# Performance work log

Measured on AMD Instinct MI355X. Metric: run time of the kernel, lower is better.

The kernel has to match this reference:

```python
import jax, jax.numpy as jnp
import numpy as np

B, T, D, U = 128, 2048, 256, 512
ALPHA = 0.001


def hard_sigmoid(x):
    return jnp.clip(0.2 * x + 0.5, 0.0, 1.0)


def setup_inputs() -> dict:
    key = jax.random.key(0)
    k1, k2, k3 = jax.random.split(key, 3)
    x = jax.random.normal(k1, (B, T, D), dtype=jnp.float32)
    h0 = jnp.zeros((B, U), dtype=jnp.float32)
    c0 = jnp.zeros((B, U), dtype=jnp.float32)
    t0 = jnp.zeros((B, U), dtype=jnp.float32)
    # glorot-ish kernels
    kernel = jax.random.normal(k2, (D, 4 * U), dtype=jnp.float32) * (1.0 / np.sqrt(D))
    recurrent_kernel = jax.random.normal(k3, (U, 4 * U), dtype=jnp.float32) * (1.0 / np.sqrt(U))
    # bias zeros with forget-gate slice = 1 (unit_forget_bias)
    bias = jnp.zeros((4 * U,), dtype=jnp.float32).at[U:2 * U].set(1.0)
    # timegate: rows = period ~ U(10,100), shift ~ U(0,1000), r_on = 0.05
    rng = np.random.RandomState(0)
    timegate_kernel = jnp.asarray(
        np.vstack((rng.uniform(10, 100, U), rng.uniform(0, 1000, U), np.zeros(U) + 0.05)),
        dtype=jnp.float32)
    return {"x": x, "h0": h0, "c0": c0, "t0": t0, "kernel": kernel,
            "recurrent_kernel": recurrent_kernel, "bias": bias,
            "timegate_kernel": timegate_kernel}


def reference(x, h0, c0, t0, kernel, recurrent_kernel, bias, timegate_kernel):
    period = timegate_kernel[0]  # [U]
    shift = timegate_kernel[1]   # [U]
    r_on = timegate_kernel[2]    # [U]

    def step(carry, x_t):
        h, c, t = carry
        t = t + 1.0
        # fused gate pre-activations: [B, 4U]
        z = x_t @ kernel + h @ recurrent_kernel + bias
        zi, zf, zc, zo = jnp.split(z, 4, axis=-1)
        i = hard_sigmoid(zi)
        f = hard_sigmoid(zf)
        c_hat = f * c + i * jnp.tanh(zc)
        o = hard_sigmoid(zo)
        h_hat = o * jnp.tanh(c_hat)
        # phased time gate
        phi = (t - shift - period * jnp.floor((t - shift) / period)) / period
        k = jnp.where(phi <= r_on * 0.5, 2.0 * phi / r_on,
                      jnp.where(phi <= r_on, 2.0 - 2.0 * phi / r_on, ALPHA * phi))
        c_new = k * c_hat + (1.0 - k) * c
        h_new = k * h_hat + (1.0 - k) * h
        return (h_new, c_new, t), h_new

    xs = jnp.swapaxes(x, 0, 1)  # [T, B, D]
    (_, _, _), hs = jax.lax.scan(step, (h0, c0, t0), xs)
    return jnp.swapaxes(hs, 0, 1)  # [B, T, U]
```

## Files before the change

kernel.cpp:

```cpp
#include <hip/hip_runtime.h>
#include <hip/hip_bf16.h>
#include <math.h>

#define B_ 128
#define T_ 2048
#define D_ 256
#define U_ 512
#define G4_ 2048
#define KT_ 768
#define ALPHA_ 0.001f

#define NGROUP 8
#define GB 16
#define NSLICE 32
#define SU 16
#define NWG (NGROUP*NSLICE)
#define NTH 256
#define BU (B_*U_)

typedef __attribute__((ext_vector_type(8))) short bf16x8;
typedef __attribute__((ext_vector_type(4))) float f32x4;
typedef __attribute__((ext_vector_type(4))) int i32x4;
typedef __attribute__((ext_vector_type(2))) int i32x2;
typedef __attribute__((ext_vector_type(4))) unsigned short us4;

#define OFF_WT 0
#define OFF_H32 (G4_*KT_*2)
#define OFF_CNT (OFF_H32 + 2*BU*4)
#define CNT_DW (NGROUP*64)

__device__ __forceinline__ unsigned short f2b(float f) {
  unsigned u = __builtin_bit_cast(unsigned, f);
  u += 0x7fffu + ((u >> 16) & 1u);
  return (unsigned short)(u >> 16);
}

__device__ __forceinline__ float ftanh(float v) {
  v = fminf(fmaxf(v, -15.f), 15.f);
  float e = __expf(2.f * v);
  return (e - 1.f) * __builtin_amdgcn_rcpf(e + 1.f);
}

__global__ void prep_kernel(const float* __restrict__ kern,
                            const float* __restrict__ rker,
                            const float* __restrict__ h0,
                            unsigned short* __restrict__ wt,
                            unsigned* __restrict__ h32,
                            unsigned* __restrict__ cnt) {
  int idx = blockIdx.x * blockDim.x + threadIdx.x;
  int stride = gridDim.x * blockDim.x;
  for (int i = idx; i < G4_ * KT_; i += stride) {
    int col = i / KT_, k = i - col * KT_;
    float v = (k < U_) ? rker[(size_t)k * G4_ + col]
                       : kern[(size_t)(k - U_) * G4_ + col];
    wt[i] = f2b(v);
  }
  for (int i = idx; i < BU; i += stride) {
    h32[i] = ((unsigned)f2b(h0[i]) << 16);
    h32[BU + i] = 0xFFFFu;
  }
  for (int i = idx; i < CNT_DW; i += stride) cnt[i] = 0u;
}

#define LOAD8()                                                        \
  asm volatile(                                                        \
      "global_load_dwordx4 %0, %8, off sc0 sc1\n\t"                    \
      "global_load_dwordx4 %1, %8, off offset:1024 sc0 sc1\n\t"        \
      "global_load_dwordx4 %2, %8, off offset:2048 sc0 sc1\n\t"        \
      "global_load_dwordx4 %3, %8, off offset:3072 sc0 sc1\n\t"        \
      "global_load_dwordx4 %4, %9, off sc0 sc1\n\t"                    \
      "global_load_dwordx4 %5, %9, off offset:1024 sc0 sc1\n\t"        \
      "global_load_dwordx4 %6, %9, off offset:2048 sc0 sc1\n\t"        \
      "global_load_dwordx4 %7, %9, off offset:3072 sc0 sc1"            \
      : "=&v"(v0), "=&v"(v1), "=&v"(v2), "=&v"(v3),                    \
        "=&v"(v4), "=&v"(v5), "=&v"(v6), "=&v"(v7)                     \
      : "v"(ppoll), "v"(ppoll2));                                      \
  __builtin_amdgcn_sched_barrier(0)

#define FENCE8()                                                       \
  asm volatile("s_waitcnt vmcnt(0)"                                    \
      : "+v"(v0), "+v"(v1), "+v"(v2), "+v"(v3),                        \
        "+v"(v4), "+v"(v5), "+v"(v6), "+v"(v7));                       \
  __builtin_amdgcn_sched_barrier(0)

#define CKV(vv) ((((unsigned)(vv)[0] ^ tgv) & 0xffffu) |               \
                 (((unsigned)(vv)[1] ^ tgv) & 0xffffu) |               \
                 (((unsigned)(vv)[2] ^ tgv) & 0xffffu) |               \
                 (((unsigned)(vv)[3] ^ tgv) & 0xffffu))

#define PK(lo, hi) (int)(((unsigned)(hi) & 0xffff0000u) | ((unsigned)(lo) >> 16))

#define PACK2(vv, k)                                                         \
  { const int r_ = 4 * wv + ((k) >> 1);                                      \
    const int ba_ = (r_ * 1024 + (((k) & 1) << 9) + 8 * ln) ^ ((r_ & 7) << 4); \
    i32x2 d_ = { PK((vv)[0], (vv)[1]), PK((vv)[2], (vv)[3]) };               \
    *(i32x2*)(hdst + ba_) = d_; }

__global__ __launch_bounds__(NTH, 1) void plstm_kernel(
    const float* __restrict__ x, const float* __restrict__ h0,
    const float* __restrict__ c0, const float* __restrict__ t0,
    const float* __restrict__ bias, const float* __restrict__ tg,
    const unsigned short* __restrict__ wt,
    unsigned* h32, unsigned* cnt, float* __restrict__ out) {
  const int wg = blockIdx.x;
  const int g = wg & 7, sl = wg >> 3;
  const int b0 = g * GB, u0 = sl * SU;
  const int tid = threadIdx.x;
  const int wave = tid >> 6, lane = tid & 63;

  __shared__ unsigned short h_lds[2][GB * U_];
  __shared__ unsigned short x_lds[2][GB * D_];
  __shared__ float z_lds[2][GB][68];
  __shared__ unsigned wgarr[4];

  bf16x8 br[16], bx[8];
  {
    const int kr0 = (lane >> 4) * 8;
    const int col0 = wave * U_ + u0 + (lane & 15);
    const unsigned short* w0 = wt + (size_t)col0 * KT_;
#pragma unroll
    for (int kt = 0; kt < 16; ++kt) br[kt] = *(const bf16x8*)(w0 + kt * 32 + kr0);
#pragma unroll
    for (int kt = 0; kt < 8; ++kt)  bx[kt] = *(const bf16x8*)(w0 + U_ + kt * 32 + kr0);
  }
  const float bias_l = bias[wave * U_ + u0 + (lane & 15)];

  const int srow = tid >> 4;
  const int j = tid & 15;
  const int bb = b0 + srow;
  const int uu = u0 + j;
  float c_st = c0[bb * U_ + uu];
  float h_st = h0[bb * U_ + uu];
  const float t_0 = t0[bb * U_ + uu];
  const float per = tg[uu];
  const float shf = tg[U_ + uu];
  const float ron = tg[2 * U_ + uu];

  const int arow = lane & 15;
  const int koff = (lane >> 4) * 16;
  const int swzA = (arow & 7) << 4;
  const int swzR = (srow & 7) << 4;
  const int wv = wave, ln = lane;

  auto stage_x = [&](int t, int buf) {
    const int f0 = j * 16;
    const float* xp = x + ((size_t)bb * T_ + t) * D_ + f0;
    char* base = (char*)&x_lds[buf][0];
#pragma unroll
    for (int q = 0; q < 4; ++q) {
      float4 v = *(const float4*)(xp + q * 4);
      us4 pk = { f2b(v.x), f2b(v.y), f2b(v.z), f2b(v.w) };
      *(us4*)(base + ((srow * 512 + (f0 + q * 4) * 2) ^ swzR)) = pk;
    }
  };

  stage_x(0, 0);
  stage_x(1, 1);
  if (tid < 4) wgarr[tid] = 0u;
  __syncthreads();

  const unsigned* gslab0 = h32 + (size_t)b0 * U_;
  const int poff = wave * 2048 + lane * 4;
  unsigned* cnt_g = cnt + g * 64;

  for (int step = 0; step < T_; ++step) {
    const int par = step & 1;

    if (step > 0) {
      const unsigned tgt = 32u * (unsigned)step;
      while (__hip_atomic_load(cnt_g, __ATOMIC_RELAXED,
                               __HIP_MEMORY_SCOPE_AGENT) < tgt)
        __builtin_amdgcn_s_sleep(1);
    }

    const unsigned* ppoll = gslab0 + (size_t)par * BU + poff;
    const unsigned* ppoll2 = ppoll + 1024;
    i32x4 v0, v1, v2, v3, v4, v5, v6, v7;
    LOAD8();

    float kk;
    {
      float xx = t_0 + (float)(step + 1) - shf;
      float ph = (xx - per * floorf(xx / per)) / per;
      kk = (ph <= 0.5f * ron) ? (2.f * ph / ron)
         : ((ph <= ron) ? (2.f - 2.f * ph / ron) : (ALPHA_ * ph));
    }
    f32x4 aa = { bias_l, bias_l, bias_l, bias_l };
    f32x4 ab = { 0.f, 0.f, 0.f, 0.f };
    {
      const char* xb = (const char*)&x_lds[par][0];
#pragma unroll
      for (int kt = 0; kt < 8; ++kt) {
        bf16x8 a = *(const bf16x8*)(xb + ((arow * 512 + kt * 64 + koff) ^ swzA));
        if (kt & 1) ab = __builtin_amdgcn_mfma_f32_16x16x32_bf16(a, bx[kt], ab, 0, 0, 0);
        else        aa = __builtin_amdgcn_mfma_f32_16x16x32_bf16(a, bx[kt], aa, 0, 0, 0);
      }
    }

    const unsigned tgv = (unsigned)step;
    FENCE8();
    for (;;) {
      unsigned bad = CKV(v0) | CKV(v1) | CKV(v2) | CKV(v3) |
                     CKV(v4) | CKV(v5) | CKV(v6) | CKV(v7);
      if (!bad) break;
      __builtin_amdgcn_s_sleep(1);
      LOAD8();
      FENCE8();
    }

    {
      char* hdst = (char*)&h_lds[par][0];
      PACK2(v0, 0); PACK2(v1, 1); PACK2(v2, 2); PACK2(v3, 3);
      PACK2(v4, 4); PACK2(v5, 5); PACK2(v6, 6); PACK2(v7, 7);
    }
    __syncthreads();

    {
      const char* hbm = (const char*)&h_lds[par][0];
#pragma unroll
      for (int kt = 0; kt < 16; ++kt) {
        bf16x8 a = *(const bf16x8*)(hbm + ((arow * 1024 + kt * 64 + koff) ^ swzA));
        if (kt & 1) ab = __builtin_amdgcn_mfma_f32_16x16x32_bf16(a, br[kt], ab, 0, 0, 0);
        else        aa = __builtin_amdgcn_mfma_f32_16x16x32_bf16(a, br[kt], aa, 0, 0, 0);
      }
    }
    const f32x4 acc = aa + ab;

#pragma unroll
    for (int r2 = 0; r2 < 4; ++r2)
      z_lds[par][(lane >> 4) * 4 + r2][wave * 16 + (lane & 15)] = acc[r2];
    __syncthreads();

    float chat;
    {
      const float* zr = &z_lds[par][srow][0];
      const float zi = zr[j], zf = zr[16 + j], zc = zr[32 + j], zo = zr[48 + j];
      float ig = fminf(fmaxf(0.2f * zi + 0.5f, 0.f), 1.f);
      float fg = fminf(fmaxf(0.2f * zf + 0.5f, 0.f), 1.f);
      float og = fminf(fmaxf(0.2f * zo + 0.5f, 0.f), 1.f);
      chat = fg * c_st + ig * ftanh(zc);
      float hhat = og * ftanh(chat);
      h_st = kk * hhat + (1.f - kk) * h_st;
      unsigned hv = ((unsigned)f2b(h_st) << 16) | (unsigned)(step + 1);
      const unsigned* hp = h32 + (size_t)((step + 1) & 1) * BU + bb * U_ + uu;
      asm volatile("global_store_dword %0, %1, off sc0 sc1"
                   :: "v"(hp), "v"(hv) : "memory");
    }

    if (lane == 0) {
      unsigned old = atomicAdd(&wgarr[step & 3], 1u);
      if (old == 3u) {
        wgarr[step & 3] = 0u;
        atomicAdd(cnt_g, 1u);
      }
    }

    c_st = kk * chat + (1.f - kk) * c_st;
    out[((size_t)bb * T_ + step) * U_ + uu] = h_st;
    if (step + 2 < T_) stage_x(step + 2, par);
  }
}

extern "C" void kernel_launch(void* const* d_in, const int* in_sizes, int n_in,
                              void* d_out, int out_size, void* d_ws,
                              size_t ws_size, hipStream_t stream) {
  const float* x    = (const float*)d_in[0];
  const float* h0   = (const float*)d_in[1];
  const float* c0   = (const float*)d_in[2];
  const float* t0   = (const float*)d_in[3];
  const float* kern = (const float*)d_in[4];
  const float* rker = (const float*)d_in[5];
  const float* bias = (const float*)d_in[6];
  const float* tg   = (const float*)d_in[7];
  float* out = (float*)d_out;

  char* ws = (char*)d_ws;
  unsigned short* wt = (unsigned short*)(ws + OFF_WT);
  unsigned* h32      = (unsigned*)(ws + OFF_H32);
  unsigned* cnt      = (unsigned*)(ws + OFF_CNT);

  prep_kernel<<<1024, 256, 0, stream>>>(kern, rker, h0, wt, h32, cnt);
  plstm_kernel<<<NWG, NTH, 0, stream>>>(x, h0, c0, t0, bias, tg, wt, h32,
                                        cnt, out);
}
```

Before: 5.210 ms.

## Replace atomic group counter with per-workgroup done flags and prefetched polling

Replaces the two-level barrier with per-wave done flags stored in global memory. The old barrier used an LDS atomic inside each workgroup and then a global atomicAdd on a shared group counter. Now each wave's lane 0 writes the step number to its own slot. Each wave polls the 32 slice flags with one lane per slice, using two alternating in-flight loads, and the first poll for the next step is issued early at the end of the current step. The next-step x staging is moved to just after the h pack barrier so it overlaps the recurrent MFMA work. This trades atomic contention and serialization for more polling traffic and more complex vmcnt accounting.

```diff
diff --git a/kernel.cpp b/kernel.cpp
--- a/kernel.cpp
+++ b/kernel.cpp
@@ -26,8 +26,8 @@
 
 #define OFF_WT 0
 #define OFF_H32 (G4_*KT_*2)
-#define OFF_CNT (OFF_H32 + 2*BU*4)
-#define CNT_DW (NGROUP*64)
+#define OFF_DONE (OFF_H32 + 2*BU*4)
+#define DONE_DW (NGROUP*128)
 
 __device__ __forceinline__ unsigned short f2b(float f) {
   unsigned u = __builtin_bit_cast(unsigned, f);
@@ -46,7 +46,7 @@
                             const float* __restrict__ h0,
                             unsigned short* __restrict__ wt,
                             unsigned* __restrict__ h32,
-                            unsigned* __restrict__ cnt) {
+                            unsigned* __restrict__ done) {
   int idx = blockIdx.x * blockDim.x + threadIdx.x;
   int stride = gridDim.x * blockDim.x;
   for (int i = idx; i < G4_ * KT_; i += stride) {
@@ -59,7 +59,7 @@
     h32[i] = ((unsigned)f2b(h0[i]) << 16);
     h32[BU + i] = 0xFFFFu;
   }
-  for (int i = idx; i < CNT_DW; i += stride) cnt[i] = 0u;
+  for (int i = idx; i < DONE_DW; i += stride) done[i] = 0u;
 }
 
 #define LOAD8()                                                        \
@@ -77,10 +77,19 @@
       : "v"(ppoll), "v"(ppoll2));                                      \
   __builtin_amdgcn_sched_barrier(0)
 
-#define FENCE8()                                                       \
+#define FENCEALL()                                                     \
   asm volatile("s_waitcnt vmcnt(0)"                                    \
       : "+v"(v0), "+v"(v1), "+v"(v2), "+v"(v3),                        \
-        "+v"(v4), "+v"(v5), "+v"(v6), "+v"(v7));                       \
+        "+v"(v4), "+v"(v5), "+v"(v6), "+v"(v7), "+v"(dA), "+v"(dB));   \
+  __builtin_amdgcn_sched_barrier(0)
+
+#define POLLI(d)                                                       \
+  asm volatile("global_load_dword %0, %1, off sc0 sc1"                 \
+      : "=&v"(d) : "v"(dpoll));                                        \
+  __builtin_amdgcn_sched_barrier(0)
+
+#define WAITP()                                                        \
+  asm volatile("s_waitcnt vmcnt(1)" : "+v"(dA), "+v"(dB));             \
   __builtin_amdgcn_sched_barrier(0)
 
 #define CKV(vv) ((((unsigned)(vv)[0] ^ tgv) & 0xffffu) |               \
@@ -101,7 +110,7 @@
     const float* __restrict__ c0, const float* __restrict__ t0,
     const float* __restrict__ bias, const float* __restrict__ tg,
     const unsigned short* __restrict__ wt,
-    unsigned* h32, unsigned* cnt, float* __restrict__ out) {
+    unsigned* h32, unsigned* done, float* __restrict__ out) {
   const int wg = blockIdx.x;
   const int g = wg & 7, sl = wg >> 3;
   const int b0 = g * GB, u0 = sl * SU;
@@ -111,7 +120,6 @@
   __shared__ unsigned short h_lds[2][GB * U_];
   __shared__ unsigned short x_lds[2][GB * D_];
   __shared__ float z_lds[2][GB][68];
-  __shared__ unsigned wgarr[4];
 
   bf16x8 br[16], bx[8];
   {
@@ -156,21 +164,30 @@
 
   stage_x(0, 0);
   stage_x(1, 1);
-  if (tid < 4) wgarr[tid] = 0u;
   __syncthreads();
 
   const unsigned* gslab0 = h32 + (size_t)b0 * U_;
   const int poff = wave * 2048 + lane * 4;
-  unsigned* cnt_g = cnt + g * 64;
+  unsigned* done_g = done + g * 128;
+  const unsigned* dpoll = done_g + wave * 32 + (lane & 31);
+  const unsigned* dmine = done_g + wave * 32 + sl;
+
+  unsigned dA = 0, dB = 0;
 
   for (int step = 0; step < T_; ++step) {
     const int par = step & 1;
 
     if (step > 0) {
-      const unsigned tgt = 32u * (unsigned)step;
-      while (__hip_atomic_load(cnt_g, __ATOMIC_RELAXED,
-                               __HIP_MEMORY_SCOPE_AGENT) < tgt)
-        __builtin_amdgcn_s_sleep(1);
+      const unsigned tgt = (unsigned)step;
+      POLLI(dB);
+      for (;;) {
+        WAITP();
+        if (__all((int)(dA >= tgt))) break;
+        POLLI(dA);
+        WAITP();
+        if (__all((int)(dB >= tgt))) break;
+        POLLI(dB);
+      }
     }
 
     const unsigned* ppoll = gslab0 + (size_t)par * BU + poff;
@@ -198,14 +215,14 @@
     }
 
     const unsigned tgv = (unsigned)step;
-    FENCE8();
+    FENCEALL();
     for (;;) {
       unsigned bad = CKV(v0) | CKV(v1) | CKV(v2) | CKV(v3) |
                      CKV(v4) | CKV(v5) | CKV(v6) | CKV(v7);
       if (!bad) break;
       __builtin_amdgcn_s_sleep(1);
       LOAD8();
-      FENCE8();
+      FENCEALL();
     }
 
     {
@@ -214,6 +231,8 @@
       PACK2(v4, 4); PACK2(v5, 5); PACK2(v6, 6); PACK2(v7, 7);
     }
     __syncthreads();
+
+    if (step + 2 < T_) stage_x(step + 2, par);
 
     {
       const char* hbm = (const char*)&h_lds[par][0];
@@ -246,18 +265,15 @@
       asm volatile("global_store_dword %0, %1, off sc0 sc1"
                    :: "v"(hp), "v"(hv) : "memory");
     }
-
     if (lane == 0) {
-      unsigned old = atomicAdd(&wgarr[step & 3], 1u);
-      if (old == 3u) {
-        wgarr[step & 3] = 0u;
-        atomicAdd(cnt_g, 1u);
-      }
-    }
+      unsigned dv = (unsigned)(step + 1);
+      asm volatile("global_store_dword %0, %1, off sc0 sc1"
+                   :: "v"(dmine), "v"(dv) : "memory");
+    }
+    if (step + 1 < T_) { POLLI(dA); }
 
     c_st = kk * chat + (1.f - kk) * c_st;
     out[((size_t)bb * T_ + step) * U_ + uu] = h_st;
-    if (step + 2 < T_) stage_x(step + 2, par);
   }
 }
 
@@ -277,9 +293,9 @@
   char* ws = (char*)d_ws;
   unsigned short* wt = (unsigned short*)(ws + OFF_WT);
   unsigned* h32      = (unsigned*)(ws + OFF_H32);
-  unsigned* cnt      = (unsigned*)(ws + OFF_CNT);
-
-  prep_kernel<<<1024, 256, 0, stream>>>(kern, rker, h0, wt, h32, cnt);
+  unsigned* done     = (unsigned*)(ws + OFF_DONE);
+
+  prep_kernel<<<1024, 256, 0, stream>>>(kern, rker, h0, wt, h32, done);
   plstm_kernel<<<NWG, NTH, 0, stream>>>(x, h0, c0, t0, bias, tg, wt, h32,
-                                        cnt, out);
-}
+                                        done, out);
+}
```

Result: slower. 9.835 ms (+88.8%).

## Widen unit slices so each wave computes all four gates in registers

Applied to the files above, without the earlier changes.

Cuts the unit slices per batch group from 32 to 8 with 64 units each, so the grid drops from 256 to 64 workgroups. Each wave now holds weights for all four gates of its 16 units and runs four MFMA accumulators. The gate nonlinearities are applied straight from the accumulators, which removes the z_lds round trip and one barrier per step. The x staging for the next steps is moved earlier so it overlaps the recurrent MFMAs. In exchange, per-step MFMA work per wave grows fourfold, fewer CUs are used, and register pressure rises sharply with 96 bf16x8 weight vectors per lane.

```diff
diff --git a/kernel.cpp b/kernel.cpp
--- a/kernel.cpp
+++ b/kernel.cpp
@@ -12,8 +12,8 @@
 
 #define NGROUP 8
 #define GB 16
-#define NSLICE 32
-#define SU 16
+#define NSLICE 8
+#define SU 64
 #define NWG (NGROUP*NSLICE)
 #define NTH 256
 #define BU (B_*U_)
@@ -110,41 +110,50 @@
 
   __shared__ unsigned short h_lds[2][GB * U_];
   __shared__ unsigned short x_lds[2][GB * D_];
-  __shared__ float z_lds[2][GB][68];
   __shared__ unsigned wgarr[4];
 
-  bf16x8 br[16], bx[8];
+  bf16x8 br[4][16], bx[4][8];
+  const int uw = u0 + wave * 16 + (lane & 15);
   {
     const int kr0 = (lane >> 4) * 8;
-    const int col0 = wave * U_ + u0 + (lane & 15);
-    const unsigned short* w0 = wt + (size_t)col0 * KT_;
-#pragma unroll
-    for (int kt = 0; kt < 16; ++kt) br[kt] = *(const bf16x8*)(w0 + kt * 32 + kr0);
-#pragma unroll
-    for (int kt = 0; kt < 8; ++kt)  bx[kt] = *(const bf16x8*)(w0 + U_ + kt * 32 + kr0);
-  }
-  const float bias_l = bias[wave * U_ + u0 + (lane & 15)];
-
-  const int srow = tid >> 4;
-  const int j = tid & 15;
-  const int bb = b0 + srow;
-  const int uu = u0 + j;
-  float c_st = c0[bb * U_ + uu];
-  float h_st = h0[bb * U_ + uu];
-  const float t_0 = t0[bb * U_ + uu];
-  const float per = tg[uu];
-  const float shf = tg[U_ + uu];
-  const float ron = tg[2 * U_ + uu];
+#pragma unroll
+    for (int gq = 0; gq < 4; ++gq) {
+      const unsigned short* w0 = wt + (size_t)(gq * U_ + uw) * KT_;
+#pragma unroll
+      for (int kt = 0; kt < 16; ++kt) br[gq][kt] = *(const bf16x8*)(w0 + kt * 32 + kr0);
+#pragma unroll
+      for (int kt = 0; kt < 8; ++kt)  bx[gq][kt] = *(const bf16x8*)(w0 + U_ + kt * 32 + kr0);
+    }
+  }
+  const float bi_i = bias[0 * U_ + uw];
+  const float bi_f = bias[1 * U_ + uw];
+  const float bi_c = bias[2 * U_ + uw];
+  const float bi_o = bias[3 * U_ + uw];
+
+  const int r0 = (lane >> 4) * 4;
+  float c_st[4], h_st[4], t_0[4];
+#pragma unroll
+  for (int r2 = 0; r2 < 4; ++r2) {
+    const int bb = b0 + r0 + r2;
+    c_st[r2] = c0[bb * U_ + uw];
+    h_st[r2] = h0[bb * U_ + uw];
+    t_0[r2] = t0[bb * U_ + uw];
+  }
+  const float per = tg[uw];
+  const float shf = tg[U_ + uw];
+  const float ron = tg[2 * U_ + uw];
 
   const int arow = lane & 15;
   const int koff = (lane >> 4) * 16;
   const int swzA = (arow & 7) << 4;
+  const int wv = wave, ln = lane;
+
+  const int srow = tid >> 4;
+  const int j16 = tid & 15;
   const int swzR = (srow & 7) << 4;
-  const int wv = wave, ln = lane;
-
   auto stage_x = [&](int t, int buf) {
-    const int f0 = j * 16;
-    const float* xp = x + ((size_t)bb * T_ + t) * D_ + f0;
+    const int f0 = j16 * 16;
+    const float* xp = x + ((size_t)(b0 + srow) * T_ + t) * D_ + f0;
     char* base = (char*)&x_lds[buf][0];
 #pragma unroll
     for (int q = 0; q < 4; ++q) {
@@ -167,7 +176,7 @@
     const int par = step & 1;
 
     if (step > 0) {
-      const unsigned tgt = 32u * (unsigned)step;
+      const unsigned tgt = (unsigned)(NSLICE * step);
       while (__hip_atomic_load(cnt_g, __ATOMIC_RELAXED,
                                __HIP_MEMORY_SCOPE_AGENT) < tgt)
         __builtin_amdgcn_s_sleep(1);
@@ -178,22 +187,27 @@
     i32x4 v0, v1, v2, v3, v4, v5, v6, v7;
     LOAD8();
 
-    float kk;
-    {
-      float xx = t_0 + (float)(step + 1) - shf;
+    float kk[4];
+#pragma unroll
+    for (int r2 = 0; r2 < 4; ++r2) {
+      float xx = t_0[r2] + (float)(step + 1) - shf;
       float ph = (xx - per * floorf(xx / per)) / per;
-      kk = (ph <= 0.5f * ron) ? (2.f * ph / ron)
-         : ((ph <= ron) ? (2.f - 2.f * ph / ron) : (ALPHA_ * ph));
-    }
-    f32x4 aa = { bias_l, bias_l, bias_l, bias_l };
-    f32x4 ab = { 0.f, 0.f, 0.f, 0.f };
+      kk[r2] = (ph <= 0.5f * ron) ? (2.f * ph / ron)
+             : ((ph <= ron) ? (2.f - 2.f * ph / ron) : (ALPHA_ * ph));
+    }
+    f32x4 ai = { bi_i, bi_i, bi_i, bi_i };
+    f32x4 af = { bi_f, bi_f, bi_f, bi_f };
+    f32x4 ac = { bi_c, bi_c, bi_c, bi_c };
+    f32x4 ao = { bi_o, bi_o, bi_o, bi_o };
     {
       const char* xb = (const char*)&x_lds[par][0];
 #pragma unroll
       for (int kt = 0; kt < 8; ++kt) {
         bf16x8 a = *(const bf16x8*)(xb + ((arow * 512 + kt * 64 + koff) ^ swzA));
-        if (kt & 1) ab = __builtin_amdgcn_mfma_f32_16x16x32_bf16(a, bx[kt], ab, 0, 0, 0);
-        else        aa = __builtin_amdgcn_mfma_f32_16x16x32_bf16(a, bx[kt], aa, 0, 0, 0);
+        ai = __builtin_amdgcn_mfma_f32_16x16x32_bf16(a, bx[0][kt], ai, 0, 0, 0);
+        af = __builtin_amdgcn_mfma_f32_16x16x32_bf16(a, bx[1][kt], af, 0, 0, 0);
+        ac = __builtin_amdgcn_mfma_f32_16x16x32_bf16(a, bx[2][kt], ac, 0, 0, 0);
+        ao = __builtin_amdgcn_mfma_f32_16x16x32_bf16(a, bx[3][kt], ao, 0, 0, 0);
       }
     }
 
@@ -215,34 +229,32 @@
     }
     __syncthreads();
 
+    if (step + 2 < T_) stage_x(step + 2, par);
+
     {
       const char* hbm = (const char*)&h_lds[par][0];
 #pragma unroll
       for (int kt = 0; kt < 16; ++kt) {
         bf16x8 a = *(const bf16x8*)(hbm + ((arow * 1024 + kt * 64 + koff) ^ swzA));
-        if (kt & 1) ab = __builtin_amdgcn_mfma_f32_16x16x32_bf16(a, br[kt], ab, 0, 0, 0);
-        else        aa = __builtin_amdgcn_mfma_f32_16x16x32_bf16(a, br[kt], aa, 0, 0, 0);
+        ai = __builtin_amdgcn_mfma_f32_16x16x32_bf16(a, br[0][kt], ai, 0, 0, 0);
+        af = __builtin_amdgcn_mfma_f32_16x16x32_bf16(a, br[1][kt], af, 0, 0, 0);
+        ac = __builtin_amdgcn_mfma_f32_16x16x32_bf16(a, br[2][kt], ac, 0, 0, 0);
+        ao = __builtin_amdgcn_mfma_f32_16x16x32_bf16(a, br[3][kt], ao, 0, 0, 0);
       }
     }
-    const f32x4 acc = aa + ab;
-
-#pragma unroll
-    for (int r2 = 0; r2 < 4; ++r2)
-      z_lds[par][(lane >> 4) * 4 + r2][wave * 16 + (lane & 15)] = acc[r2];
-    __syncthreads();
-
-    float chat;
-    {
-      const float* zr = &z_lds[par][srow][0];
-      const float zi = zr[j], zf = zr[16 + j], zc = zr[32 + j], zo = zr[48 + j];
-      float ig = fminf(fmaxf(0.2f * zi + 0.5f, 0.f), 1.f);
-      float fg = fminf(fmaxf(0.2f * zf + 0.5f, 0.f), 1.f);
-      float og = fminf(fmaxf(0.2f * zo + 0.5f, 0.f), 1.f);
-      chat = fg * c_st + ig * ftanh(zc);
-      float hhat = og * ftanh(chat);
-      h_st = kk * hhat + (1.f - kk) * h_st;
-      unsigned hv = ((unsigned)f2b(h_st) << 16) | (unsigned)(step + 1);
-      const unsigned* hp = h32 + (size_t)((step + 1) & 1) * BU + bb * U_ + uu;
+
+    float chat[4];
+#pragma unroll
+    for (int r2 = 0; r2 < 4; ++r2) {
+      float ig = fminf(fmaxf(0.2f * ai[r2] + 0.5f, 0.f), 1.f);
+      float fg = fminf(fmaxf(0.2f * af[r2] + 0.5f, 0.f), 1.f);
+      float og = fminf(fmaxf(0.2f * ao[r2] + 0.5f, 0.f), 1.f);
+      chat[r2] = fg * c_st[r2] + ig * ftanh(ac[r2]);
+      float hhat = og * ftanh(chat[r2]);
+      h_st[r2] = kk[r2] * hhat + (1.f - kk[r2]) * h_st[r2];
+      unsigned hv = ((unsigned)f2b(h_st[r2]) << 16) | (unsigned)(step + 1);
+      const unsigned* hp = h32 + (size_t)((step + 1) & 1) * BU
+                         + (b0 + r0 + r2) * U_ + uw;
       asm volatile("global_store_dword %0, %1, off sc0 sc1"
                    :: "v"(hp), "v"(hv) : "memory");
     }
@@ -255,9 +267,11 @@
       }
     }
 
-    c_st = kk * chat + (1.f - kk) * c_st;
-    out[((size_t)bb * T_ + step) * U_ + uu] = h_st;
-    if (step + 2 < T_) stage_x(step + 2, par);
+#pragma unroll
+    for (int r2 = 0; r2 < 4; ++r2) {
+      c_st[r2] = kk[r2] * chat[r2] + (1.f - kk[r2]) * c_st[r2];
+      out[((size_t)(b0 + r0 + r2) * T_ + step) * U_ + uw] = h_st[r2];
+    }
   }
 }
 
```

After: 12.73 ms. 144% more time.

## Replace atomic step counter with per-slice done flags and move x staging earlier

Applied to the files above, without the earlier changes.

The per-group barrier previously had every workgroup atomically increment one shared counter and poll it until it reached 32 times the step. Now each workgroup writes its own step number into a dedicated flag slot with a plain store, and waiters load all 32 slots in parallel (one per lane) and check them with a wave-wide vote. This removes serialized atomic contention on a single address. Staging of the next x tile also moves to right after the h barrier, so it overlaps with the MFMA work rather than trailing at the end of the step, at the cost of possibly delaying the gate computation.

```diff
diff --git a/kernel.cpp b/kernel.cpp
--- a/kernel.cpp
+++ b/kernel.cpp
@@ -26,8 +26,8 @@
 
 #define OFF_WT 0
 #define OFF_H32 (G4_*KT_*2)
-#define OFF_CNT (OFF_H32 + 2*BU*4)
-#define CNT_DW (NGROUP*64)
+#define OFF_DONE (OFF_H32 + 2*BU*4)
+#define DONE_DW (NGROUP*64)
 
 __device__ __forceinline__ unsigned short f2b(float f) {
   unsigned u = __builtin_bit_cast(unsigned, f);
@@ -46,7 +46,7 @@
                             const float* __restrict__ h0,
                             unsigned short* __restrict__ wt,
                             unsigned* __restrict__ h32,
-                            unsigned* __restrict__ cnt) {
+                            unsigned* __restrict__ done) {
   int idx = blockIdx.x * blockDim.x + threadIdx.x;
   int stride = gridDim.x * blockDim.x;
   for (int i = idx; i < G4_ * KT_; i += stride) {
@@ -59,7 +59,7 @@
     h32[i] = ((unsigned)f2b(h0[i]) << 16);
     h32[BU + i] = 0xFFFFu;
   }
-  for (int i = idx; i < CNT_DW; i += stride) cnt[i] = 0u;
+  for (int i = idx; i < DONE_DW; i += stride) done[i] = 0u;
 }
 
 #define LOAD8()                                                        \
@@ -101,7 +101,7 @@
     const float* __restrict__ c0, const float* __restrict__ t0,
     const float* __restrict__ bias, const float* __restrict__ tg,
     const unsigned short* __restrict__ wt,
-    unsigned* h32, unsigned* cnt, float* __restrict__ out) {
+    unsigned* h32, unsigned* done, float* __restrict__ out) {
   const int wg = blockIdx.x;
   const int g = wg & 7, sl = wg >> 3;
   const int b0 = g * GB, u0 = sl * SU;
@@ -161,16 +161,23 @@
 
   const unsigned* gslab0 = h32 + (size_t)b0 * U_;
   const int poff = wave * 2048 + lane * 4;
-  unsigned* cnt_g = cnt + g * 64;
+  unsigned* done_g = done + g * 64;
+  const unsigned* dslot = done_g + (lane & 31);
+  const unsigned* dmine = done_g + sl;
 
   for (int step = 0; step < T_; ++step) {
     const int par = step & 1;
 
     if (step > 0) {
-      const unsigned tgt = 32u * (unsigned)step;
-      while (__hip_atomic_load(cnt_g, __ATOMIC_RELAXED,
-                               __HIP_MEMORY_SCOPE_AGENT) < tgt)
+      const unsigned tgt = (unsigned)step;
+      for (;;) {
+        unsigned d;
+        asm volatile("global_load_dword %0, %1, off sc0 sc1\n\t"
+                     "s_waitcnt vmcnt(0)"
+                     : "=v"(d) : "v"(dslot) : "memory");
+        if (__all((int)(d >= tgt))) break;
         __builtin_amdgcn_s_sleep(1);
+      }
     }
 
     const unsigned* ppoll = gslab0 + (size_t)par * BU + poff;
@@ -214,6 +221,8 @@
       PACK2(v4, 4); PACK2(v5, 5); PACK2(v6, 6); PACK2(v7, 7);
     }
     __syncthreads();
+
+    if (step + 2 < T_) stage_x(step + 2, par);
 
     {
       const char* hbm = (const char*)&h_lds[par][0];
@@ -251,13 +260,14 @@
       unsigned old = atomicAdd(&wgarr[step & 3], 1u);
       if (old == 3u) {
         wgarr[step & 3] = 0u;
-        atomicAdd(cnt_g, 1u);
+        unsigned dv = (unsigned)(step + 1);
+        asm volatile("global_store_dword %0, %1, off sc0 sc1"
+                     :: "v"(dmine), "v"(dv) : "memory");
       }
     }
 
     c_st = kk * chat + (1.f - kk) * c_st;
     out[((size_t)bb * T_ + step) * U_ + uu] = h_st;
-    if (step + 2 < T_) stage_x(step + 2, par);
   }
 }
 
@@ -277,9 +287,9 @@
   char* ws = (char*)d_ws;
   unsigned short* wt = (unsigned short*)(ws + OFF_WT);
   unsigned* h32      = (unsigned*)(ws + OFF_H32);
-  unsigned* cnt      = (unsigned*)(ws + OFF_CNT);
-
-  prep_kernel<<<1024, 256, 0, stream>>>(kern, rker, h0, wt, h32, cnt);
+  unsigned* done     = (unsigned*)(ws + OFF_DONE);
+
+  prep_kernel<<<1024, 256, 0, stream>>>(kern, rker, h0, wt, h32, done);
   plstm_kernel<<<NWG, NTH, 0, stream>>>(x, h0, c0, t0, bias, tg, wt, h32,
-                                        cnt, out);
-}
+                                        done, out);
+}
```

Result: slower. 6.929 ms (+33.0%).
